# Kernel optimization log

Measured on AMD Instinct MI355X. Metric: run time of the kernel, lower is better.

Reference implementation:

```python
import jax, jax.numpy as jnp
import numpy as np

POOL_SIZE = 7
NUM_ROIS = 600
H, W, C = 96, 96, 1024


def setup_inputs() -> dict:
    key = jax.random.key(0)
    k_img, k_xy, k_wh = jax.random.split(key, 3)
    img = jax.random.normal(k_img, (1, H, W, C), dtype=jnp.float32)
    # (x, y) top-left corners and (w, h) sizes, all integer feature-map coords
    xy = jax.random.randint(k_xy, (1, NUM_ROIS, 2), 0, 64, dtype=jnp.int32)
    wh = jax.random.randint(k_wh, (1, NUM_ROIS, 2), 4, 36, dtype=jnp.int32)
    rois = jnp.concatenate([xy, wh], axis=-1)  # (1, num_rois, 4) as (x, y, w, h)
    return {"img": img, "rois": rois}


def _pool_one_roi(img2d, roi):
    """img2d: (H, W, C) float; roi: (4,) int32 (x, y, w, h).
    Reproduces tf.image.resize_images (bilinear, align_corners=False, TF1
    semantics: src = dst * in/out) applied to the crop img[y:y+h, x:x+w],
    without materializing the dynamic-shape crop."""
    x, y, w, h = roi[0], roi[1], roi[2], roi[3]
    w = jnp.maximum(w, 1)
    h = jnp.maximum(h, 1)
    out_idx = jnp.arange(POOL_SIZE, dtype=jnp.float32)
    # source coords within the crop
    in_y = out_idx * (h.astype(jnp.float32) / POOL_SIZE)
    in_x = out_idx * (w.astype(jnp.float32) / POOL_SIZE)
    y0 = jnp.floor(in_y).astype(jnp.int32)
    x0 = jnp.floor(in_x).astype(jnp.int32)
    y1 = jnp.minimum(y0 + 1, h - 1)
    x1 = jnp.minimum(x0 + 1, w - 1)
    fy = (in_y - y0.astype(jnp.float32))[:, None, None]  # (P,1,1)
    fx = (in_x - x0.astype(jnp.float32))[None, :, None]  # (1,P,1)
    # map crop-local indices into the full image, clamp for safety
    r0 = jnp.clip(y + y0, 0, H - 1)
    r1 = jnp.clip(y + y1, 0, H - 1)
    c0 = jnp.clip(x + x0, 0, W - 1)
    c1 = jnp.clip(x + x1, 0, W - 1)
    top = img2d[r0[:, None], c0[None, :]] * (1.0 - fx) + img2d[r0[:, None], c1[None, :]] * fx
    bot = img2d[r1[:, None], c0[None, :]] * (1.0 - fx) + img2d[r1[:, None], c1[None, :]] * fx
    return top * (1.0 - fy) + bot * fy  # (P, P, C)


def reference(img, rois):
    img2d = img[0]          # (H, W, C)
    rois2d = rois[0]        # (num_rois, 4)
    out = jax.vmap(_pool_one_roi, in_axes=(None, 0))(img2d, rois2d)
    return out[None]        # (1, num_rois, P, P, C)
```

## Files before the change

### kernel.cpp

```cpp
#include <hip/hip_runtime.h>

#define POOL 7
#define NUM_ROIS 600
#define IMG_H 96
#define IMG_W 96
#define IMG_C 1024

typedef float v4f __attribute__((ext_vector_type(4)));

__global__ __launch_bounds__(256) void roi_pool_kernel(
    const float* __restrict__ img,
    const int* __restrict__ rois,
    float* __restrict__ out)
{
    const int b   = blockIdx.x;
    const int xcd = b & 7;
    const int j   = b >> 3;
    const int py  = j % POOL;
    const int k   = j / POOL;
    const int roi = k * 8 + xcd;

    const int4 r = *(const int4*)(rois + roi * 4);
    const int x = r.x;
    const int y = r.y;
    const int w = max(r.z, 1);
    const int h = max(r.w, 1);

    const float sy = (float)h / (float)POOL;
    const float sx = (float)w / (float)POOL;

    const float in_y = (float)py * sy;
    const int y0 = (int)floorf(in_y);
    const int y1 = min(y0 + 1, h - 1);
    const float fy = in_y - (float)y0;
    const float gy = 1.0f - fy;
    const int R0 = min(max(y + y0, 0), IMG_H - 1);
    const int R1 = min(max(y + y1, 0), IMG_H - 1);

    const int ch = threadIdx.x * 4;
    const float* row0 = img + (size_t)R0 * IMG_W * IMG_C + ch;
    const float* row1 = img + (size_t)R1 * IMG_W * IMG_C + ch;
    float* outp = out + ((size_t)roi * POOL * POOL + (size_t)py * POOL) * IMG_C + ch;

#pragma unroll
    for (int px = 0; px < POOL; ++px) {
        const float in_x = (float)px * sx;
        const int x0 = (int)floorf(in_x);
        const int x1 = min(x0 + 1, w - 1);
        const float fx = in_x - (float)x0;
        const float gx = 1.0f - fx;
        const int C0 = min(max(x + x0, 0), IMG_W - 1);
        const int C1 = min(max(x + x1, 0), IMG_W - 1);

        const v4f v00 = *(const v4f*)(row0 + (size_t)C0 * IMG_C);
        const v4f v01 = *(const v4f*)(row0 + (size_t)C1 * IMG_C);
        const v4f v10 = *(const v4f*)(row1 + (size_t)C0 * IMG_C);
        const v4f v11 = *(const v4f*)(row1 + (size_t)C1 * IMG_C);

        const v4f o = (v00 * gx + v01 * fx) * gy + (v10 * gx + v11 * fx) * fy;

        __builtin_nontemporal_store(o, (v4f*)(outp + (size_t)px * IMG_C));
    }
}

extern "C" void kernel_launch(void* const* d_in, const int* in_sizes, int n_in,
                              void* d_out, int out_size, void* d_ws, size_t ws_size,
                              hipStream_t stream) {
    const float* img  = (const float*)d_in[0];
    const int*   rois = (const int*)d_in[1];
    float*       out  = (float*)d_out;

    const int nblocks = NUM_ROIS * POOL;
    roi_pool_kernel<<<nblocks, 256, 0, stream>>>(img, rois, out);
}
```

Before: 181.8 us.

## Sort ROIs by spatial Morton bin so each XCD handles nearby ROIs

Adds a small single-block pre-pass that buckets ROIs by Morton-ordered 8x8 spatial bin of their top-left corner and writes a permutation into workspace. The main kernel then assigns each XCD a contiguous slice of the sorted ROIs, so blocks on the same XCD read overlapping image regions. The aim is better L2 reuse per XCD, given that the 37.7 MB image exceeds a single XCD's L2. In exchange it adds an extra kernel launch and a serial dependency before the pooling kernel, plus one indirection load per block.

```diff
diff --git a/kernel.cpp b/kernel.cpp
--- a/kernel.cpp
+++ b/kernel.cpp
@@ -8,17 +8,50 @@
 
 typedef float v4f __attribute__((ext_vector_type(4)));
 
+__global__ __launch_bounds__(640) void bin_rois_kernel(
+    const int* __restrict__ rois, int* __restrict__ perm)
+{
+    __shared__ int cnt[64];
+    __shared__ int base[64];
+    const int t = threadIdx.x;
+    if (t < 64) cnt[t] = 0;
+    __syncthreads();
+
+    int mybin = 0;
+    if (t < NUM_ROIS) {
+        const int x = rois[t * 4 + 0];
+        const int y = rois[t * 4 + 1];
+        const int bx = min(max(x, 0), 63) >> 3;
+        const int by = min(max(y, 0), 63) >> 3;
+        mybin = (bx & 1) | ((by & 1) << 1) | ((bx & 2) << 1) |
+                ((by & 2) << 2) | ((bx & 4) << 2) | ((by & 4) << 3);
+        atomicAdd(&cnt[mybin], 1);
+    }
+    __syncthreads();
+    if (t == 0) {
+        int s = 0;
+        for (int i = 0; i < 64; ++i) { base[i] = s; s += cnt[i]; cnt[i] = 0; }
+    }
+    __syncthreads();
+    if (t < NUM_ROIS) {
+        const int pos = base[mybin] + atomicAdd(&cnt[mybin], 1);
+        perm[pos] = t;
+    }
+}
+
 __global__ __launch_bounds__(256) void roi_pool_kernel(
     const float* __restrict__ img,
     const int* __restrict__ rois,
+    const int* __restrict__ perm,
     float* __restrict__ out)
 {
-    const int b   = blockIdx.x;
-    const int xcd = b & 7;
-    const int j   = b >> 3;
-    const int py  = j % POOL;
-    const int k   = j / POOL;
-    const int roi = k * 8 + xcd;
+    const int g   = blockIdx.x;
+    const int xcd = g & 7;
+    const int i   = g >> 3;
+    const int py  = i % POOL;
+    const int loc = i / POOL;
+    const int pos = xcd * (NUM_ROIS / 8) + loc;
+    const int roi = perm[pos];
 
     const int4 r = *(const int4*)(rois + roi * 4);
     const int x = r.x;
@@ -69,7 +102,8 @@
     const float* img  = (const float*)d_in[0];
     const int*   rois = (const int*)d_in[1];
     float*       out  = (float*)d_out;
+    int*         perm = (int*)d_ws;
 
-    const int nblocks = NUM_ROIS * POOL;
-    roi_pool_kernel<<<nblocks, 256, 0, stream>>>(img, rois, out);
+    bin_rois_kernel<<<1, 640, 0, stream>>>(rois, perm);
+    roi_pool_kernel<<<NUM_ROIS * POOL, 256, 0, stream>>>(img, rois, perm, out);
 }
```

Result: faster. 175.4 us (-3.6%).
